# Kernel tuning notes

Hardware: AMD Instinct MI355X
Metric: run time of the kernel (lower is better)

The kernel has to match this reference:

```python
import jax, jax.numpy as jnp
import numpy as np

EMBED = 1024
HEADS = 16
HEAD_DIM = EMBED // HEADS


def setup_inputs() -> dict:
    key = jax.random.key(0)
    k1, k2, k3, k4, k5 = jax.random.split(key, 5)
    B, S, E = 4, 2048, EMBED
    scale = 1.0 / np.sqrt(E)
    return {
        "tensor": jax.random.normal(k1, (B, S, E), dtype=jnp.float32),
        "in_proj_w": jax.random.normal(k2, (3 * E, E), dtype=jnp.float32) * scale,
        "in_proj_b": jax.random.normal(k3, (3 * E,), dtype=jnp.float32) * 0.02,
        "out_proj_w": jax.random.normal(k4, (E, E), dtype=jnp.float32) * scale,
        "out_proj_b": jax.random.normal(k5, (E,), dtype=jnp.float32) * 0.02,
        "causal_mask": 1,
    }


def reference(tensor, in_proj_w, in_proj_b, out_proj_w, out_proj_b, causal_mask):
    B, S, E = tensor.shape
    H, D = HEADS, HEAD_DIM
    # fused qkv projection (torch Linear: x @ W.T + b)
    qkv = tensor @ in_proj_w.T + in_proj_b  # [B, S, 3E]
    q, k, v = jnp.split(qkv, 3, axis=-1)
    # [B, S, E] -> [B, H, S, D]
    q = q.reshape(B, S, H, D).transpose(0, 2, 1, 3)
    k = k.reshape(B, S, H, D).transpose(0, 2, 1, 3)
    v = v.reshape(B, S, H, D).transpose(0, 2, 1, 3)
    scores = jnp.einsum("bhqd,bhkd->bhqk", q, k)  # [B, H, S, S]
    if causal_mask:
        mask = jnp.triu(jnp.ones((S, S), dtype=bool), k=1)
        scores = jnp.where(mask, -jnp.inf, scores)
    scores = scores / np.sqrt(D).astype(np.float32)
    attn = jax.nn.softmax(scores, axis=-1)
    out = jnp.einsum("bhqk,bhkd->bhqd", attn, v)  # [B, H, S, D]
    out = out.transpose(0, 2, 1, 3).reshape(B, S, E)
    return out @ out_proj_w.T + out_proj_b
```

## Files before the change

### kernel.cpp

```cpp
#include <hip/hip_runtime.h>
#include <hip/hip_bf16.h>

#define B_  4
#define S_  2048
#define E_  1024
#define H_  16
#define D_  64
#define M_  (B_*S_)
#define N3_ (3*E_)

typedef __bf16 bf16;
typedef bf16  bf16x4 __attribute__((ext_vector_type(4)));
typedef bf16  bf16x8 __attribute__((ext_vector_type(8)));
typedef float f32x4  __attribute__((ext_vector_type(4)));

#define SC2 0.18033688011112043f

__device__ __forceinline__ f32x4 mfma16(bf16x8 a, bf16x8 b, f32x4 c) {
    return __builtin_amdgcn_mfma_f32_16x16x32_bf16(a, b, c, 0, 0, 0);
}

typedef const __attribute__((address_space(1))) void* gas_t;
typedef __attribute__((address_space(3))) void* las_t;
__device__ __forceinline__ void gl_lds16(const void* g, void* l) {
    __builtin_amdgcn_global_load_lds((gas_t)g, (las_t)l, 16, 0, 0);
}

#define WAIT_LGKM0() __builtin_amdgcn_s_waitcnt(0xC07F)

__global__ __launch_bounds__(256) void cvt_all(const float* __restrict__ x,
                                               const float* __restrict__ w_in,
                                               const float* __restrict__ w_out,
                                               bf16* __restrict__ Xbf,
                                               bf16* __restrict__ Wqkv,
                                               bf16* __restrict__ Wo) {
    const int n1 = M_ * E_ / 4, n2 = N3_ * E_ / 4, n3 = E_ * E_ / 4;
    int i = blockIdx.x * blockDim.x + threadIdx.x;
    const float* src; bf16* dst; int j;
    if (i < n1)           { src = x;     dst = Xbf;  j = i; }
    else if (i < n1 + n2) { src = w_in;  dst = Wqkv; j = i - n1; }
    else if (i < n1 + n2 + n3) { src = w_out; dst = Wo; j = i - n1 - n2; }
    else return;
    float4 v = *(const float4*)(src + (size_t)j * 4);
    bf16x4 o;
    o[0] = (bf16)v.x; o[1] = (bf16)v.y; o[2] = (bf16)v.z; o[3] = (bf16)v.w;
    *(bf16x4*)(dst + (size_t)j * 4) = o;
}

__global__ __launch_bounds__(256) void gemm_qkv(const bf16* __restrict__ X,
                                                const bf16* __restrict__ W,
                                                const float* __restrict__ bias,
                                                bf16* __restrict__ QKV,
                                                bf16* __restrict__ Vt) {
    __shared__ __align__(16) bf16 As[128 * 64];
    __shared__ __align__(16) bf16 Bs[128 * 64];
    const int t = threadIdx.x;
    const int wav = t >> 6, lane = t & 63, quad = lane >> 4, l15 = lane & 15;
    const int m0 = blockIdx.y * 128, n0 = blockIdx.x * 128;
    const int wr = (wav >> 1) * 64, wc = (wav & 1) * 64;
    const int srow = t >> 3;
    const int swz  = ((t & 7) ^ (srow & 7)) * 8;
    const bool isV = (n0 >= 2 * E_);

    const bf16* Ablk = X + (size_t)m0 * E_;
    const bf16* Bblk = W + (size_t)n0 * E_;
    f32x4 acc[4][4] = {};

    for (int kk = 0; kk < E_; kk += 64) {
        __syncthreads();
        #pragma unroll
        for (int ps = 0; ps < 4; ++ps) {
            gl_lds16(Ablk + (size_t)(srow + ps * 32) * E_ + kk + swz, As + (size_t)(t + ps * 256) * 8);
            gl_lds16(Bblk + (size_t)(srow + ps * 32) * E_ + kk + swz, Bs + (size_t)(t + ps * 256) * 8);
        }
        __syncthreads();
        #pragma unroll
        for (int ks = 0; ks < 2; ++ks) {
            bf16x8 af[4], bw[4];
            #pragma unroll
            for (int i = 0; i < 4; ++i) {
                const int ra = wr + i * 16 + l15;
                const int rb = wc + i * 16 + l15;
                const int cx = ((ks * 4 + quad) ^ (l15 & 7)) * 8;
                af[i] = *(const bf16x8*)&As[ra * 64 + cx];
                bw[i] = *(const bf16x8*)&Bs[rb * 64 + cx];
            }
            if (!isV) {
                #pragma unroll
                for (int i = 0; i < 4; ++i)
                    #pragma unroll
                    for (int j = 0; j < 4; ++j)
                        acc[i][j] = mfma16(af[i], bw[j], acc[i][j]);
            } else {
                #pragma unroll
                for (int i = 0; i < 4; ++i)
                    #pragma unroll
                    for (int j = 0; j < 4; ++j)
                        acc[i][j] = mfma16(bw[i], af[j], acc[i][j]);
            }
        }
    }
    if (!isV) {
        #pragma unroll
        for (int i = 0; i < 4; ++i)
            #pragma unroll
            for (int j = 0; j < 4; ++j)
                #pragma unroll
                for (int r = 0; r < 4; ++r) {
                    int mg = m0 + wr + i * 16 + quad * 4 + r;
                    int ng = n0 + wc + j * 16 + l15;
                    float v = acc[i][j][r] + bias[ng];
                    int which = ng >> 10, rem = ng & 1023;
                    if (which == 0) v *= SC2;
                    int h = rem >> 6, d = rem & 63;
                    int b = mg >> 11, s = mg & 2047;
                    QKV[(size_t)which * (B_ * H_ * S_ * D_) +
                        (((size_t)(b * H_ + h) * S_ + s) * D_ + d)] = (bf16)v;
                }
    } else {
        #pragma unroll
        for (int i = 0; i < 4; ++i)
            #pragma unroll
            for (int j = 0; j < 4; ++j)
                #pragma unroll
                for (int r = 0; r < 4; ++r) {
                    int ng = n0 + wc + i * 16 + quad * 4 + r;
                    int mg = m0 + wr + j * 16 + l15;
                    float v = acc[i][j][r] + bias[ng];
                    int rem = ng & 1023;
                    int h = rem >> 6, d = rem & 63;
                    int b = mg >> 11, s = mg & 2047;
                    Vt[(((size_t)(b * H_ + h) * D_ + d) * S_) + s] = (bf16)v;
                }
    }
}

#define LDK 72
#define LDP 72

__global__ __launch_bounds__(256, 4) void attn5(const bf16* __restrict__ Q,
                                                const bf16* __restrict__ K,
                                                const bf16* __restrict__ Vt,
                                                bf16* __restrict__ O) {
    __shared__ __align__(16) bf16 Ks[64 * LDK];
    __shared__ __align__(16) bf16 Vs[64 * LDK];
    __shared__ __align__(16) bf16 Ps[4][16 * LDP];

    const int t = threadIdx.x;
    const int wav = t >> 6, lane = t & 63, quad = lane >> 4, l15 = lane & 15;
    const int p  = blockIdx.x >> 6;
    const int bh = blockIdx.x & 63;

    const bf16* Qb = Q  + (size_t)bh * S_ * D_;
    const bf16* Kb = K  + (size_t)bh * S_ * D_;
    const bf16* Vb = Vt + (size_t)bh * (size_t)D_ * S_;

    const int rk = t >> 2;
    const int ck = (t & 3) * 16;
    bf16* Pw = &Ps[wav][0];

    const int b = bh >> 4, h = bh & 15;

    bf16x8 stK0, stK1, stV0, stV1;

    #pragma unroll 1
    for (int phase = 0; phase < 2; ++phase) {
        const int qb  = phase ? (31 - p) : p;
        const int q0w = qb * 64 + wav * 16;
        const int qg  = q0w + l15;

        bf16x8 qf0 = *(const bf16x8*)&Qb[(size_t)(q0w + l15) * D_ + quad * 8];
        bf16x8 qf1 = *(const bf16x8*)&Qb[(size_t)(q0w + l15) * D_ + 32 + quad * 8];

        f32x4 oacc[4] = {};
        float mst = -3e38f, lst = 0.f;

        const int niter = qb + 1;
        stK0 = *(const bf16x8*)&Kb[(size_t)rk * D_ + ck];
        stK1 = *(const bf16x8*)&Kb[(size_t)rk * D_ + ck + 8];
        stV0 = *(const bf16x8*)&Vb[(size_t)rk * S_ + ck];
        stV1 = *(const bf16x8*)&Vb[(size_t)rk * S_ + ck + 8];

        #pragma unroll 1
        for (int it = 0; it < niter; ++it) {
            const int key0 = it * 64;
            __builtin_amdgcn_s_barrier();
            *(bf16x8*)&Ks[rk * LDK + ck]     = stK0;
            *(bf16x8*)&Ks[rk * LDK + ck + 8] = stK1;
            *(bf16x8*)&Vs[rk * LDK + ck]     = stV0;
            *(bf16x8*)&Vs[rk * LDK + ck + 8] = stV1;
            if (it + 1 < niter) {
                const int kn = key0 + 64;
                stK0 = *(const bf16x8*)&Kb[(size_t)(kn + rk) * D_ + ck];
                stK1 = *(const bf16x8*)&Kb[(size_t)(kn + rk) * D_ + ck + 8];
                stV0 = *(const bf16x8*)&Vb[(size_t)rk * S_ + kn + ck];
                stV1 = *(const bf16x8*)&Vb[(size_t)rk * S_ + kn + ck + 8];
            }
            WAIT_LGKM0();
            __builtin_amdgcn_s_barrier();

            f32x4 sacc[4];
            #pragma unroll
            for (int mt = 0; mt < 4; ++mt) {
                const int krow = mt * 16 + l15;
                bf16x8 kf0 = *(const bf16x8*)&Ks[krow * LDK + quad * 8];
                bf16x8 kf1 = *(const bf16x8*)&Ks[krow * LDK + 32 + quad * 8];
                f32x4 a = {};
                a = mfma16(kf0, qf0, a);
                a = mfma16(kf1, qf1, a);
                sacc[mt] = a;
            }

            float rmax = -3e38f;
            #pragma unroll
            for (int mt = 0; mt < 4; ++mt) {
                if (key0 + mt * 16 + 15 <= q0w) {
                    #pragma unroll
                    for (int r = 0; r < 4; ++r) rmax = fmaxf(rmax, sacc[mt][r]);
                } else {
                    #pragma unroll
                    for (int r = 0; r < 4; ++r) {
                        int key = key0 + mt * 16 + quad * 4 + r;
                        float v = (key > qg) ? -3e38f : sacc[mt][r];
                        sacc[mt][r] = v;
                        rmax = fmaxf(rmax, v);
                    }
                }
            }
            rmax = fmaxf(rmax, __shfl_xor(rmax, 16));
            rmax = fmaxf(rmax, __shfl_xor(rmax, 32));

            const float mn = fmaxf(mst, rmax);
            const float al = __builtin_amdgcn_exp2f(mst - mn);
            float rsum = 0.f;
            #pragma unroll
            for (int mt = 0; mt < 4; ++mt)
                #pragma unroll
                for (int r = 0; r < 4; ++r) {
                    float pv = __builtin_amdgcn_exp2f(sacc[mt][r] - mn);
                    sacc[mt][r] = pv;
                    rsum += pv;
                }
            rsum += __shfl_xor(rsum, 16);
            rsum += __shfl_xor(rsum, 32);
            lst = lst * al + rsum;
            mst = mn;

            #pragma unroll
            for (int mt = 0; mt < 4; ++mt) {
                bf16x4 pk;
                #pragma unroll
                for (int r = 0; r < 4; ++r) pk[r] = (bf16)sacc[mt][r];
                *(bf16x4*)&Pw[l15 * LDP + mt * 16 + quad * 4] = pk;
            }

            if (__ballot(al < 1.0f) != 0ull) {
                #pragma unroll
                for (int rr = 0; rr < 4; ++rr) {
                    float alr = __shfl(al, quad * 4 + rr);
                    #pragma unroll
                    for (int nt = 0; nt < 4; ++nt) oacc[nt][rr] *= alr;
                }
            }

            bf16x8 pf0 = *(const bf16x8*)&Pw[l15 * LDP + quad * 8];
            bf16x8 pf1 = *(const bf16x8*)&Pw[l15 * LDP + 32 + quad * 8];
            #pragma unroll
            for (int nt = 0; nt < 4; ++nt) {
                const int vrow = nt * 16 + l15;
                bf16x8 vf0 = *(const bf16x8*)&Vs[vrow * LDK + quad * 8];
                bf16x8 vf1 = *(const bf16x8*)&Vs[vrow * LDK + 32 + quad * 8];
                oacc[nt] = mfma16(pf0, vf0, oacc[nt]);
                oacc[nt] = mfma16(pf1, vf1, oacc[nt]);
            }
        }

        const float linv = 1.0f / lst;
        #pragma unroll
        for (int rr = 0; rr < 4; ++rr) {
            float li = __shfl(linv, quad * 4 + rr);
            const int q = q0w + quad * 4 + rr;
            #pragma unroll
            for (int nt = 0; nt < 4; ++nt)
                O[((size_t)b * S_ + q) * E_ + h * D_ + nt * 16 + l15] =
                    (bf16)(oacc[nt][rr] * li);
        }
    }
}

__global__ __launch_bounds__(256) void gemm_out(const bf16* __restrict__ A,
                                                const bf16* __restrict__ W,
                                                const float* __restrict__ bias,
                                                float* __restrict__ out) {
    __shared__ __align__(16) bf16 As[128 * 64];
    __shared__ __align__(16) bf16 Bs[128 * 64];
    const int t = threadIdx.x;
    const int wav = t >> 6, lane = t & 63, quad = lane >> 4, l15 = lane & 15;
    const int m0 = blockIdx.y * 128, n0 = blockIdx.x * 128;
    const int wr = (wav >> 1) * 64, wc = (wav & 1) * 64;
    const int srow = t >> 3;
    const int swz  = ((t & 7) ^ (srow & 7)) * 8;

    const bf16* Ablk = A + (size_t)m0 * E_;
    const bf16* Bblk = W + (size_t)n0 * E_;
    f32x4 acc[4][4] = {};

    for (int kk = 0; kk < E_; kk += 64) {
        __syncthreads();
        #pragma unroll
        for (int ps = 0; ps < 4; ++ps) {
            gl_lds16(Ablk + (size_t)(srow + ps * 32) * E_ + kk + swz, As + (size_t)(t + ps * 256) * 8);
            gl_lds16(Bblk + (size_t)(srow + ps * 32) * E_ + kk + swz, Bs + (size_t)(t + ps * 256) * 8);
        }
        __syncthreads();
        #pragma unroll
        for (int ks = 0; ks < 2; ++ks) {
            bf16x8 af[4], bw[4];
            #pragma unroll
            for (int i = 0; i < 4; ++i) {
                const int ra = wr + i * 16 + l15;
                const int rb = wc + i * 16 + l15;
                const int cx = ((ks * 4 + quad) ^ (l15 & 7)) * 8;
                af[i] = *(const bf16x8*)&As[ra * 64 + cx];
                bw[i] = *(const bf16x8*)&Bs[rb * 64 + cx];
            }
            #pragma unroll
            for (int i = 0; i < 4; ++i)
                #pragma unroll
                for (int j = 0; j < 4; ++j)
                    acc[i][j] = mfma16(af[i], bw[j], acc[i][j]);
        }
    }
    #pragma unroll
    for (int i = 0; i < 4; ++i)
        #pragma unroll
        for (int j = 0; j < 4; ++j)
            #pragma unroll
            for (int r = 0; r < 4; ++r) {
                int mg = m0 + wr + i * 16 + quad * 4 + r;
                int ng = n0 + wc + j * 16 + l15;
                out[(size_t)mg * E_ + ng] = acc[i][j][r] + bias[ng];
            }
}

extern "C" void kernel_launch(void* const* d_in, const int* in_sizes, int n_in,
                              void* d_out, int out_size, void* d_ws, size_t ws_size,
                              hipStream_t stream) {
    const float* x     = (const float*)d_in[0];
    const float* w_in  = (const float*)d_in[1];
    const float* b_in  = (const float*)d_in[2];
    const float* w_out = (const float*)d_in[3];
    const float* b_out = (const float*)d_in[4];
    float* out = (float*)d_out;

    char* ws = (char*)d_ws;
    bf16* Xbf  = (bf16*)ws; ws += (size_t)M_ * E_ * 2;
    bf16* Wqkv = (bf16*)ws; ws += (size_t)N3_ * E_ * 2;
    bf16* Wo   = (bf16*)ws; ws += (size_t)E_ * E_ * 2;
    bf16* QKV  = (bf16*)ws; ws += (size_t)2 * B_ * H_ * S_ * D_ * 2;
    bf16* Vt   = (bf16*)ws; ws += (size_t)B_ * H_ * S_ * D_ * 2;
    bf16* Obf  = Xbf;

    const int nCvt = (M_ * E_ + N3_ * E_ + E_ * E_) / 4;
    cvt_all<<<(nCvt + 255) / 256, 256, 0, stream>>>(x, w_in, w_out, Xbf, Wqkv, Wo);

    gemm_qkv<<<dim3(N3_ / 128, M_ / 128), 256, 0, stream>>>(Xbf, Wqkv, b_in, QKV, Vt);

    bf16* Qp = QKV;
    bf16* Kp = QKV + (size_t)B_ * H_ * S_ * D_;

    attn5<<<dim3(16 * B_ * H_), 256, 0, stream>>>(Qp, Kp, Vt, Obf);

    gemm_out<<<dim3(E_ / 128, M_ / 128), 256, 0, stream>>>(Obf, Wo, b_out, out);
}
```

Baseline: 257.4 us.

## Double-buffer attention K/V tiles via direct global-to-LDS loads with XOR swizzle

```diff
diff --git a/kernel.cpp b/kernel.cpp
--- a/kernel.cpp
+++ b/kernel.cpp
@@ -26,7 +26,8 @@
     __builtin_amdgcn_global_load_lds((gas_t)g, (las_t)l, 16, 0, 0);
 }
 
-#define WAIT_LGKM0() __builtin_amdgcn_s_waitcnt(0xC07F)
+#define WAITCNT_VM4() __builtin_amdgcn_s_waitcnt(0x0F74)
+#define WAITCNT_VM0() __builtin_amdgcn_s_waitcnt(0x0F70)
 
 __global__ __launch_bounds__(256) void cvt_all(const float* __restrict__ x,
                                                const float* __restrict__ w_in,
@@ -135,16 +136,13 @@
     }
 }
 
-#define LDK 72
-#define LDP 72
-
-__global__ __launch_bounds__(256, 4) void attn5(const bf16* __restrict__ Q,
+__global__ __launch_bounds__(256, 4) void attn6(const bf16* __restrict__ Q,
                                                 const bf16* __restrict__ K,
                                                 const bf16* __restrict__ Vt,
                                                 bf16* __restrict__ O) {
-    __shared__ __align__(16) bf16 Ks[64 * LDK];
-    __shared__ __align__(16) bf16 Vs[64 * LDK];
-    __shared__ __align__(16) bf16 Ps[4][16 * LDP];
+    __shared__ __align__(16) bf16 Ks[2][64 * 64];
+    __shared__ __align__(16) bf16 Vs[2][64 * 64];
+    __shared__ __align__(16) bf16 Ps[4][16 * 64];
 
     const int t = threadIdx.x;
     const int wav = t >> 6, lane = t & 63, quad = lane >> 4, l15 = lane & 15;
@@ -155,56 +153,61 @@
     const bf16* Kb = K  + (size_t)bh * S_ * D_;
     const bf16* Vb = Vt + (size_t)bh * (size_t)D_ * S_;
 
-    const int rk = t >> 2;
-    const int ck = (t & 3) * 16;
+    const int srow = t >> 3;
+    const int swz  = ((t & 7) ^ (srow & 7)) * 8;
     bf16* Pw = &Ps[wav][0];
+    const int pswz = l15 & 7;
 
     const int b = bh >> 4, h = bh & 15;
-
-    bf16x8 stK0, stK1, stV0, stV1;
 
     #pragma unroll 1
     for (int phase = 0; phase < 2; ++phase) {
         const int qb  = phase ? (31 - p) : p;
         const int q0w = qb * 64 + wav * 16;
         const int qg  = q0w + l15;
+        const int niter = qb + 1;
+
+        __builtin_amdgcn_s_barrier();
+        gl_lds16(Kb + (size_t)srow * D_ + swz,        &Ks[0][(size_t)t * 8]);
+        gl_lds16(Kb + (size_t)(srow + 32) * D_ + swz, &Ks[0][(size_t)(t + 256) * 8]);
+        gl_lds16(Vb + (size_t)srow * S_ + swz,        &Vs[0][(size_t)t * 8]);
+        gl_lds16(Vb + (size_t)(srow + 32) * S_ + swz, &Vs[0][(size_t)(t + 256) * 8]);
 
         bf16x8 qf0 = *(const bf16x8*)&Qb[(size_t)(q0w + l15) * D_ + quad * 8];
         bf16x8 qf1 = *(const bf16x8*)&Qb[(size_t)(q0w + l15) * D_ + 32 + quad * 8];
 
         f32x4 oacc[4] = {};
         float mst = -3e38f, lst = 0.f;
-
-        const int niter = qb + 1;
-        stK0 = *(const bf16x8*)&Kb[(size_t)rk * D_ + ck];
-        stK1 = *(const bf16x8*)&Kb[(size_t)rk * D_ + ck + 8];
-        stV0 = *(const bf16x8*)&Vb[(size_t)rk * S_ + ck];
-        stV1 = *(const bf16x8*)&Vb[(size_t)rk * S_ + ck + 8];
 
         #pragma unroll 1
         for (int it = 0; it < niter; ++it) {
             const int key0 = it * 64;
+            const int cur = it & 1;
+            const bf16* Kc = &Ks[cur][0];
+            const bf16* Vc = &Vs[cur][0];
+
             __builtin_amdgcn_s_barrier();
-            *(bf16x8*)&Ks[rk * LDK + ck]     = stK0;
-            *(bf16x8*)&Ks[rk * LDK + ck + 8] = stK1;
-            *(bf16x8*)&Vs[rk * LDK + ck]     = stV0;
-            *(bf16x8*)&Vs[rk * LDK + ck + 8] = stV1;
             if (it + 1 < niter) {
                 const int kn = key0 + 64;
-                stK0 = *(const bf16x8*)&Kb[(size_t)(kn + rk) * D_ + ck];
-                stK1 = *(const bf16x8*)&Kb[(size_t)(kn + rk) * D_ + ck + 8];
-                stV0 = *(const bf16x8*)&Vb[(size_t)rk * S_ + kn + ck];
-                stV1 = *(const bf16x8*)&Vb[(size_t)rk * S_ + kn + ck + 8];
-            }
-            WAIT_LGKM0();
+                bf16* Kn = &Ks[1 - cur][0];
+                bf16* Vn = &Vs[1 - cur][0];
+                gl_lds16(Kb + (size_t)(kn + srow) * D_ + swz,        Kn + (size_t)t * 8);
+                gl_lds16(Kb + (size_t)(kn + srow + 32) * D_ + swz,   Kn + (size_t)(t + 256) * 8);
+                gl_lds16(Vb + (size_t)srow * S_ + kn + swz,          Vn + (size_t)t * 8);
+                gl_lds16(Vb + (size_t)(srow + 32) * S_ + kn + swz,   Vn + (size_t)(t + 256) * 8);
+                WAITCNT_VM4();
+            } else {
+                WAITCNT_VM0();
+            }
             __builtin_amdgcn_s_barrier();
 
             f32x4 sacc[4];
             #pragma unroll
             for (int mt = 0; mt < 4; ++mt) {
                 const int krow = mt * 16 + l15;
-                bf16x8 kf0 = *(const bf16x8*)&Ks[krow * LDK + quad * 8];
-                bf16x8 kf1 = *(const bf16x8*)&Ks[krow * LDK + 32 + quad * 8];
+                const int sw = krow & 7;
+                bf16x8 kf0 = *(const bf16x8*)&Kc[krow * 64 + ((quad ^ sw) * 8)];
+                bf16x8 kf1 = *(const bf16x8*)&Kc[krow * 64 + (((4 + quad) ^ sw) * 8)];
                 f32x4 a = {};
                 a = mfma16(kf0, qf0, a);
                 a = mfma16(kf1, qf1, a);
@@ -251,7 +254,8 @@
                 bf16x4 pk;
                 #pragma unroll
                 for (int r = 0; r < 4; ++r) pk[r] = (bf16)sacc[mt][r];
-                *(bf16x4*)&Pw[l15 * LDP + mt * 16 + quad * 4] = pk;
+                const int pc = ((mt * 2 + (quad >> 1)) ^ pswz) * 8 + (quad & 1) * 4;
+                *(bf16x4*)&Pw[l15 * 64 + pc] = pk;
             }
 
             if (__ballot(al < 1.0f) != 0ull) {
@@ -263,13 +267,14 @@
                 }
             }
 
-            bf16x8 pf0 = *(const bf16x8*)&Pw[l15 * LDP + quad * 8];
-            bf16x8 pf1 = *(const bf16x8*)&Pw[l15 * LDP + 32 + quad * 8];
+            bf16x8 pf0 = *(const bf16x8*)&Pw[l15 * 64 + ((quad ^ pswz) * 8)];
+            bf16x8 pf1 = *(const bf16x8*)&Pw[l15 * 64 + (((4 + quad) ^ pswz) * 8)];
             #pragma unroll
             for (int nt = 0; nt < 4; ++nt) {
                 const int vrow = nt * 16 + l15;
-                bf16x8 vf0 = *(const bf16x8*)&Vs[vrow * LDK + quad * 8];
-                bf16x8 vf1 = *(const bf16x8*)&Vs[vrow * LDK + 32 + quad * 8];
+                const int sw = vrow & 7;
+                bf16x8 vf0 = *(const bf16x8*)&Vc[vrow * 64 + ((quad ^ sw) * 8)];
+                bf16x8 vf1 = *(const bf16x8*)&Vc[vrow * 64 + (((4 + quad) ^ sw) * 8)];
                 oacc[nt] = mfma16(pf0, vf0, oacc[nt]);
                 oacc[nt] = mfma16(pf1, vf1, oacc[nt]);
             }
@@ -369,7 +374,7 @@
     bf16* Qp = QKV;
     bf16* Kp = QKV + (size_t)B_ * H_ * S_ * D_;
 
-    attn5<<<dim3(16 * B_ * H_), 256, 0, stream>>>(Qp, Kp, Vt, Obf);
+    attn6<<<dim3(16 * B_ * H_), 256, 0, stream>>>(Qp, Kp, Vt, Obf);
 
     gemm_out<<<dim3(E_ / 128, M_ / 128), 256, 0, stream>>>(Obf, Wo, b_out, out);
 }
```

After: 249.4 us. 1.03x faster.
